# Optimization experiments

Measured on AMD Instinct MI355X. Metric: run time of the kernel, lower is better.

## Reference

```python
import jax, jax.numpy as jnp
import numpy as np

N = 50000; E = 800000; G = 64
HID = 128; HEADS = 4; HC = HID // HEADS
L = 3; RESID_FREQ = 2
EPS = 1e-5; SLOPE = 0.2


def setup_inputs() -> dict:
    key = jax.random.key(0)
    ks = jax.random.split(key, 16)
    s = 1.0 / np.sqrt(HID)
    f = jnp.float32
    return {
        "x": jax.random.normal(ks[0], (N, HID), f),
        "edge_index": jax.random.randint(ks[1], (2, E), 0, N, dtype=jnp.int32),
        "batch": jnp.sort(jax.random.randint(ks[2], (N,), 0, G, dtype=jnp.int32)),
        "w_in1": jax.random.normal(ks[3], (HID, HID), f) * s,
        "b_in1": jnp.zeros((HID,), f),
        "w_in2": jax.random.normal(ks[4], (HID, HID), f) * s,
        "b_in2": jnp.zeros((HID,), f),
        "gat_w": jax.random.normal(ks[5], (L, HID, HID), f) * s,
        "gat_att_src": jax.random.normal(ks[6], (L, HEADS, HC), f) * s,
        "gat_att_dst": jax.random.normal(ks[7], (L, HEADS, HC), f) * s,
        "gat_b": jnp.zeros((L, HID), f),
        "gcn_w": jax.random.normal(ks[8], (L, HID, HID), f) * s,
        "gcn_b": jnp.zeros((L, HID), f),
        "norm_w": jnp.ones((L, HID), f),
        "norm_b": jnp.zeros((L, HID), f),
        "norm_ms": jnp.ones((L, HID), f),
        "skip_w": jax.random.normal(ks[9], (L, HID, HID), f) * s,
        "skip_b": jnp.zeros((L, HID), f),
        "w_h1": jax.random.normal(ks[10], (HID, HID), f) * s,
        "b_h1": jnp.zeros((HID,), f),
        "w_h2": jax.random.normal(ks[11], (HID, HID // 2), f) * s,
        "b_h2": jnp.zeros((HID // 2,), f),
        "w_h3": jax.random.normal(ks[12], (HID // 2, 1), f) * s,
        "b_h3": jnp.zeros((1,), f),
        "edge_w_param": jnp.ones((1,), f),
    }


def _gat(x, src, dst, w, a_src, a_dst, b):
    # PyG GATConv (eval): lin -> per-edge additive attention -> edge softmax over dst -> scatter-sum
    h = (x @ w).reshape(N, HEADS, HC)
    sc_src = jnp.sum(h * a_src, axis=-1)  # [N, H]
    sc_dst = jnp.sum(h * a_dst, axis=-1)
    alpha = jax.nn.leaky_relu(sc_src[src] + sc_dst[dst], SLOPE)  # [Ef, H]
    amax = jax.ops.segment_max(alpha, dst, num_segments=N)  # every node has a self-loop
    ex = jnp.exp(alpha - amax[dst])
    denom = jax.ops.segment_sum(ex, dst, num_segments=N)
    coef = ex / (denom[dst] + 1e-16)
    out = jax.ops.segment_sum(h[src] * coef[:, :, None], dst, num_segments=N)
    return out.reshape(N, HID) + b


def _gcn(x, src, dst, ew, w, b):
    # PyG GCNConv with improved=True (self-loop weight 2.0 already in ew): sym-normalized SpMM
    deg = jax.ops.segment_sum(ew, dst, num_segments=N)
    dinv = jnp.where(deg > 0, jax.lax.rsqrt(deg), 0.0)
    norm = dinv[src] * ew * dinv[dst]
    h = x @ w
    return jax.ops.segment_sum(h[src] * norm[:, None], dst, num_segments=N) + b


def _graph_norm(x, batch, w, b, ms):
    cnt = jax.ops.segment_sum(jnp.ones((N, 1), x.dtype), batch, num_segments=G)
    cnt = jnp.maximum(cnt, 1.0)
    mean = jax.ops.segment_sum(x, batch, num_segments=G) / cnt
    out = x - mean[batch] * ms
    var = jax.ops.segment_sum(out * out, batch, num_segments=G) / cnt
    return out / jnp.sqrt(var[batch] + EPS) * w + b


def reference(x, edge_index, batch, w_in1, b_in1, w_in2, b_in2, gat_w, gat_att_src,
              gat_att_dst, gat_b, gcn_w, gcn_b, norm_w, norm_b, norm_ms, skip_w,
              skip_b, w_h1, b_h1, w_h2, b_h2, w_h3, b_h3, edge_w_param):
    # undirected: concat reversed edges; then self-loops (added by both GAT and GCN convs)
    loop = jnp.arange(N, dtype=edge_index.dtype)
    src = jnp.concatenate([edge_index[0], edge_index[1], loop])
    dst = jnp.concatenate([edge_index[1], edge_index[0], loop])
    ew = jnp.concatenate([
        edge_w_param[0] * jnp.ones((2 * E,), x.dtype),
        2.0 * jnp.ones((N,), x.dtype),  # improved=True self-loop fill value
    ])
    h = jax.nn.relu(x @ w_in1 + b_in1) @ w_in2 + b_in2
    for i in range(L):
        prev = h
        g1 = _gat(h, src, dst, gat_w[i], gat_att_src[i], gat_att_dst[i], gat_b[i])
        g2 = _gcn(h, src, dst, ew, gcn_w[i], gcn_b[i])
        h = jax.nn.elu(_graph_norm(g1 + g2, batch, norm_w[i], norm_b[i], norm_ms[i]))
        if i % RESID_FREQ == 0:
            h = h + prev @ skip_w[i] + skip_b[i]
    p = jax.nn.relu(h @ w_h1 + b_h1)
    p = jax.nn.relu(p @ w_h2 + b_h2)
    return jax.nn.sigmoid(p @ w_h3 + b_h3).reshape(-1)
```

## Files before the change

kernel.cpp:

```cpp
#include <hip/hip_runtime.h>
#include <hip/hip_fp16.h>

typedef unsigned int uint;
typedef unsigned short ushort;
typedef __attribute__((ext_vector_type(8))) short short8;
typedef __attribute__((ext_vector_type(4))) float f32x4;
typedef __attribute__((ext_vector_type(2))) float f32x2;

#define N_NODES 50000
#define N_EDGES 800000
#define EREAL   (2 * N_EDGES)
#define ETOT    (2 * N_EDGES + N_NODES)
#define NG      64
#define NBKT    256
#define MAXB    10240
#define EPB     8192
#define NBK1    ((EREAL + EPB - 1) / EPB)
#define AROW    640

__device__ __forceinline__ short f2bf(float f) {
  uint u = __float_as_uint(f);
  u += 0x7fffu + ((u >> 16) & 1u);
  return (short)(u >> 16);
}
__device__ __forceinline__ float bf2f(short s) {
  return __uint_as_float(((uint)(ushort)s) << 16);
}
__device__ __forceinline__ uint packbf(float a, float b) {
  return (uint)(ushort)f2bf(a) | ((uint)(ushort)f2bf(b) << 16);
}
__device__ __forceinline__ uint pkh2(float a, float b) {
  __half2 h = __floats2half2_rn(a, b);
  return *(uint*)&h;
}
__device__ __forceinline__ float2 uph2(uint u) {
  __half2 h = *(__half2*)&u;
  return __half22float2(h);
}

__global__ __launch_bounds__(256) void bucket_k(const int* __restrict__ ei,
                                                int* __restrict__ gfill,
                                                uint* __restrict__ est) {
  __shared__ int hist[NBKT];
  __shared__ int scan_[NBKT];
  __shared__ int cur[NBKT];
  __shared__ int claim[NBKT];
  __shared__ int wsum[4];
  __shared__ uint stage[EPB];
  const int tid = threadIdx.x;
  hist[tid] = 0;
  __syncthreads();
  const int e0 = blockIdx.x * EPB;
  const int ecnt = min(EPB, EREAL - e0);
  for (int i = tid; i < ecnt; i += 256) {
    int e = e0 + i;
    int d = (e < N_EDGES) ? ei[N_EDGES + e] : ei[e - N_EDGES];
    atomicAdd(&hist[d >> 8], 1);
  }
  __syncthreads();
  {
    int v = hist[tid];
    int lane = tid & 63, wid = tid >> 6;
    int x = v;
#pragma unroll
    for (int d = 1; d < 64; d <<= 1) {
      int t = __shfl_up(x, d, 64);
      if (lane >= d) x += t;
    }
    if (lane == 63) wsum[wid] = x;
    __syncthreads();
    int woff = 0;
#pragma unroll
    for (int j = 0; j < 4; ++j) if (j < wid) woff += wsum[j];
    scan_[tid] = woff + x - v;
    cur[tid] = woff + x - v;
    claim[tid] = atomicAdd(&gfill[tid], v);
  }
  __syncthreads();
  for (int i = tid; i < ecnt; i += 256) {
    int e = e0 + i;
    int s = ei[e];
    int d = (e < N_EDGES) ? ei[N_EDGES + e] : ei[e - N_EDGES];
    int p = atomicAdd(&cur[d >> 8], 1);
    stage[p] = (uint)s | ((uint)d << 16);
  }
  __syncthreads();
  for (int p = tid; p < ecnt; p += 256) {
    uint en = stage[p];
    int b = en >> 24;
    int gpos = claim[b] + (p - scan_[b]);
    est[(size_t)b * MAXB + gpos] = en;
  }
}

__global__ __launch_bounds__(256) void group_k(const int* __restrict__ gfill,
                                               const uint* __restrict__ est,
                                               const float* __restrict__ ewp,
                                               int* __restrict__ csrc,
                                               int* __restrict__ rbeg,
                                               int* __restrict__ rend,
                                               float* __restrict__ dinv) {
  __shared__ int hist[NBKT];
  __shared__ int cursor[NBKT];
  __shared__ int wsum[4];
  __shared__ int bsum[4];
  const int b = blockIdx.x;
  const int tid = threadIdx.x;
  const int lane = tid & 63, wid = tid >> 6;
  const int cnt = gfill[b];
  {
    int vv = (tid < b) ? gfill[tid] : 0;
#pragma unroll
    for (int off = 32; off; off >>= 1) vv += __shfl_xor(vv, off, 64);
    if (lane == 0) bsum[wid] = vv;
  }
  hist[tid] = 0;
  __syncthreads();
  const int gb = bsum[0] + bsum[1] + bsum[2] + bsum[3] + b * 256;
  const uint* basep = est + (size_t)b * MAXB;
  for (int i = tid; i < cnt; i += 256)
    atomicAdd(&hist[(basep[i] >> 16) & 255], 1);
  __syncthreads();
  int v = hist[tid];
  int x = v;
#pragma unroll
  for (int d = 1; d < 64; d <<= 1) {
    int t = __shfl_up(x, d, 64);
    if (lane >= d) x += t;
  }
  if (lane == 63) wsum[wid] = x;
  __syncthreads();
  int woff = 0;
#pragma unroll
  for (int j = 0; j < 4; ++j) if (j < wid) woff += wsum[j];
  int excl = woff + x - v;
  cursor[tid] = excl + tid + 1;
  int node = b * 256 + tid;
  if (node < N_NODES) {
    int rs = gb + excl + tid;
    rbeg[node] = rs;
    rend[node] = rs + v + 1;
    csrc[rs] = node | (int)0x80000000;
    float deg = ewp[0] * (float)v + 2.0f;
    dinv[node] = (deg > 0.f) ? rsqrtf(deg) : 0.f;
  }
  __syncthreads();
  for (int i = tid; i < cnt; i += 256) {
    uint en = basep[i];
    int dlow = (en >> 16) & 255;
    int slot = atomicAdd(&cursor[dlow], 1);
    csrc[gb + slot] = (int)(en & 0xffffu);
  }
}

__global__ __launch_bounds__(256) void prepall_k(const float* __restrict__ w_in1,
                                                 const float* __restrict__ w_in2,
                                                 const float* __restrict__ gat_w,
                                                 const float* __restrict__ gcn_w,
                                                 const float* __restrict__ skip_w,
                                                 const float* __restrict__ w_h1,
                                                 const float* __restrict__ w_h2,
                                                 const float* __restrict__ asrc,
                                                 const float* __restrict__ adst,
                                                 const float* __restrict__ gat_b,
                                                 const float* __restrict__ gcn_b,
                                                 const int* __restrict__ batch,
                                                 short* __restrict__ WT0,
                                                 short* __restrict__ WT1,
                                                 short* __restrict__ WTL2,
                                                 short* __restrict__ WTS,
                                                 short* __restrict__ WTH1,
                                                 short* __restrict__ WTH2,
                                                 short* __restrict__ ATTW,
                                                 float* __restrict__ BSUM,
                                                 int* __restrict__ gcnt) {
  __shared__ int lb[NG + 1];
  const int tid = threadIdx.x;
  if (blockIdx.x == 48) {
    for (int t = tid; t < 3072; t += 256) {
      int l = t >> 10, rem = t & 1023;
      int r = rem >> 7, k = rem & 127;
      int hd = r & 3;
      const float* av = (r < 4) ? (asrc + l * 128 + hd * 32) : (adst + l * 128 + hd * 32);
      const float* wrow = gat_w + (size_t)l * 16384 + k * 128 + hd * 32;
      float s = 0.f;
#pragma unroll
      for (int c = 0; c < 32; ++c) s = fmaf(wrow[c], av[c], s);
      ATTW[(size_t)l * 2048 + r * 128 + k] = f2bf(s);
    }
    for (int t = tid; t < 3072; t += 256)
      ATTW[(size_t)(t >> 10) * 2048 + 1024 + (t & 1023)] = 0;
    for (int t = tid; t < 384; t += 256) {
      int l = t >> 7, c = t & 127;
      BSUM[t] = gat_b[l * 128 + c] + gcn_b[l * 128 + c];
    }
    return;
  }
  if (blockIdx.x == 49) {
    int g = tid;
    if (g <= NG) {
      int lo = 0, hi = N_NODES;
      while (lo < hi) {
        int mid = (lo + hi) >> 1;
        if (batch[mid] < g) lo = mid + 1; else hi = mid;
      }
      lb[g] = lo;
    }
    __syncthreads();
    if (g < NG) gcnt[g] = lb[g + 1] - lb[g];
    return;
  }
  int mat = blockIdx.x >> 2, qr = blockIdx.x & 3;
  const float* src; short* dst; int ncol = 128, dstride = 128, doff = 0;
  switch (mat) {
    case 0:  src = w_in1; dst = WT0; break;
    case 1:  src = w_in2; dst = WT1; break;
    case 2: case 3: case 4:
      src = gat_w + (size_t)(mat - 2) * 16384; dst = WTL2 + (size_t)(mat - 2) * 32768;
      dstride = 256; break;
    case 5: case 6: case 7:
      src = gcn_w + (size_t)(mat - 5) * 16384; dst = WTL2 + (size_t)(mat - 5) * 32768;
      dstride = 256; doff = 128; break;
    case 8:  src = skip_w;             dst = WTS;         break;
    case 9:  src = skip_w + 2 * 16384; dst = WTS + 16384; break;
    case 10: src = w_h1; dst = WTH1; break;
    default: src = w_h2; dst = WTH2; ncol = 64; break;
  }
  int total = 128 * ncol, chunk = total / 4;
  for (int d = qr * chunk + tid; d < (qr + 1) * chunk; d += 256) {
    int col = d >> 7, k = d & 127;
    dst[col * dstride + doff + k] = f2bf(src[k * ncol + col]);
  }
}

template <int NCOL, int RELU, int F32OUT, int NORM>
__global__ __launch_bounds__(256) void bgemm_k(const short* __restrict__ A,
                                               const short* __restrict__ WT,
                                               const float* __restrict__ bias,
                                               const short* __restrict__ gb_,
                                               const int* __restrict__ batch,
                                               const int* __restrict__ gcnt,
                                               const float* __restrict__ gsum,
                                               const float* __restrict__ nw,
                                               const float* __restrict__ nb_,
                                               const float* __restrict__ nms,
                                               short* __restrict__ outb,
                                               float* __restrict__ outf, int M) {
  constexpr int NT = NCOL / 16;
  const int lane = threadIdx.x & 63;
  const int wid = threadIdx.x >> 6;
  const int mbase = blockIdx.x * 64 + wid * 16;
  const int l15 = lane & 15, q = lane >> 4;
  int arow = mbase + l15; if (arow > M - 1) arow = M - 1;
  const short* ap = A + (size_t)arow * 128 + q * 8;
  const short* bp = WT + (size_t)l15 * 128 + q * 8;
  f32x4 acc[NT];
#pragma unroll
  for (int t = 0; t < NT; ++t) acc[t] = (f32x4)0.f;
#pragma unroll
  for (int c = 0; c < 4; ++c) {
    short8 av = *(const short8*)(ap + c * 32);
#pragma unroll
    for (int t = 0; t < NT; ++t) {
      short8 bv = *(const short8*)(bp + (size_t)t * 16 * 128 + c * 32);
      acc[t] = __builtin_amdgcn_mfma_f32_16x16x32_bf16(av, bv, acc[t], 0, 0, 0);
    }
  }
#pragma unroll
  for (int t = 0; t < NT; ++t) {
    int col = t * 16 + l15;
    float bb = bias ? bias[col] : 0.f;
#pragma unroll
    for (int r = 0; r < 4; ++r) {
      int row = mbase + q * 4 + r;
      if (row < M) {
        float v = acc[t][r] + bb;
        if (NORM) {
          int b = batch[row];
          float cinv = 1.0f / fmaxf((float)gcnt[b], 1.0f);
          float mean = gsum[b * 256 + col] * cinv;
          float msq  = gsum[b * 256 + 128 + col] * cinv;
          float ms = nms[col];
          float var = fmaxf(msq - (2.0f * ms - ms * ms) * mean * mean, 0.f);
          float g = bf2f(gb_[(size_t)row * AROW + col]);
          float tn = (g - mean * ms) * rsqrtf(var + 1e-5f) * nw[col] + nb_[col];
          tn = (tn > 0.f) ? tn : (__expf(tn) - 1.0f);
          v += tn;
        }
        if (RELU) v = v > 0.f ? v : 0.f;
        if (F32OUT) outf[(size_t)row * NCOL + col] = v;
        else        outb[(size_t)row * NCOL + col] = f2bf(v);
      }
    }
  }
}

__global__ __launch_bounds__(256) void mlp2_k(const float* __restrict__ x,
                                              const short* __restrict__ WT0,
                                              const float* __restrict__ b1,
                                              const short* __restrict__ WT1,
                                              const float* __restrict__ b2,
                                              short* __restrict__ outb, int M) {
  __shared__ short sh[64][136];
  const int lane = threadIdx.x & 63;
  const int wid = threadIdx.x >> 6;
  const int mbase = blockIdx.x * 64 + wid * 16;
  const int l15 = lane & 15, q = lane >> 4;
  int arow = mbase + l15; if (arow > M - 1) arow = M - 1;
  f32x4 acc[8];
#pragma unroll
  for (int t = 0; t < 8; ++t) acc[t] = (f32x4)0.f;
#pragma unroll
  for (int c = 0; c < 4; ++c) {
    const float* apf = x + (size_t)arow * 128 + q * 8 + c * 32;
    float4 fa = *(const float4*)apf;
    float4 fb = *(const float4*)(apf + 4);
    uint4 all = make_uint4(packbf(fa.x, fa.y), packbf(fa.z, fa.w),
                           packbf(fb.x, fb.y), packbf(fb.z, fb.w));
    short8 av = *(short8*)&all;
    const short* bp = WT0 + (size_t)l15 * 128 + q * 8 + c * 32;
#pragma unroll
    for (int t = 0; t < 8; ++t) {
      short8 bv = *(const short8*)(bp + (size_t)t * 16 * 128);
      acc[t] = __builtin_amdgcn_mfma_f32_16x16x32_bf16(av, bv, acc[t], 0, 0, 0);
    }
  }
#pragma unroll
  for (int t = 0; t < 8; ++t) {
    int col = t * 16 + l15;
    float bb = b1[col];
#pragma unroll
    for (int r = 0; r < 4; ++r) {
      float v = acc[t][r] + bb;
      sh[wid * 16 + q * 4 + r][col] = f2bf(v > 0.f ? v : 0.f);
    }
  }
  __syncthreads();
  f32x4 acc2[8];
#pragma unroll
  for (int t = 0; t < 8; ++t) acc2[t] = (f32x4)0.f;
  const short* ap2 = &sh[wid * 16 + l15][0] + q * 8;
#pragma unroll
  for (int c = 0; c < 4; ++c) {
    short8 av = *(const short8*)(ap2 + c * 32);
    const short* bp = WT1 + (size_t)l15 * 128 + q * 8 + c * 32;
#pragma unroll
    for (int t = 0; t < 8; ++t) {
      short8 bv = *(const short8*)(bp + (size_t)t * 16 * 128);
      acc2[t] = __builtin_amdgcn_mfma_f32_16x16x32_bf16(av, bv, acc2[t], 0, 0, 0);
    }
  }
#pragma unroll
  for (int t = 0; t < 8; ++t) {
    int col = t * 16 + l15;
    float bb = b2[col];
#pragma unroll
    for (int r = 0; r < 4; ++r) {
      int row = mbase + q * 4 + r;
      if (row < M) outb[(size_t)row * 128 + col] = f2bf(acc2[t][r] + bb);
    }
  }
}

__global__ __launch_bounds__(256) void head_k(const short* __restrict__ h,
                                              const short* __restrict__ WTH1,
                                              const float* __restrict__ b1,
                                              const short* __restrict__ WTH2,
                                              const float* __restrict__ b2,
                                              const float* __restrict__ w3,
                                              const float* __restrict__ b3,
                                              float* __restrict__ out, int M) {
  __shared__ short sh[64][136];
  const int lane = threadIdx.x & 63;
  const int wid = threadIdx.x >> 6;
  const int mbase = blockIdx.x * 64 + wid * 16;
  const int l15 = lane & 15, q = lane >> 4;
  int arow = mbase + l15; if (arow > M - 1) arow = M - 1;
  const short* ap = h + (size_t)arow * 128 + q * 8;
  f32x4 acc[8];
#pragma unroll
  for (int t = 0; t < 8; ++t) acc[t] = (f32x4)0.f;
#pragma unroll
  for (int c = 0; c < 4; ++c) {
    short8 av = *(const short8*)(ap + c * 32);
    const short* bp = WTH1 + (size_t)l15 * 128 + q * 8 + c * 32;
#pragma unroll
    for (int t = 0; t < 8; ++t) {
      short8 bv = *(const short8*)(bp + (size_t)t * 16 * 128);
      acc[t] = __builtin_amdgcn_mfma_f32_16x16x32_bf16(av, bv, acc[t], 0, 0, 0);
    }
  }
#pragma unroll
  for (int t = 0; t < 8; ++t) {
    int col = t * 16 + l15;
    float bb = b1[col];
#pragma unroll
    for (int r = 0; r < 4; ++r) {
      float v = acc[t][r] + bb;
      sh[wid * 16 + q * 4 + r][col] = f2bf(v > 0.f ? v : 0.f);
    }
  }
  __syncthreads();
  f32x4 p2[4];
#pragma unroll
  for (int t = 0; t < 4; ++t) p2[t] = (f32x4)0.f;
  const short* ap2 = &sh[wid * 16 + l15][0] + q * 8;
#pragma unroll
  for (int c = 0; c < 4; ++c) {
    short8 av = *(const short8*)(ap2 + c * 32);
    const short* bp = WTH2 + (size_t)l15 * 128 + q * 8 + c * 32;
#pragma unroll
    for (int t = 0; t < 4; ++t) {
      short8 bv = *(const short8*)(bp + (size_t)t * 16 * 128);
      p2[t] = __builtin_amdgcn_mfma_f32_16x16x32_bf16(av, bv, p2[t], 0, 0, 0);
    }
  }
  float w3v[4];
#pragma unroll
  for (int t = 0; t < 4; ++t) w3v[t] = w3[t * 16 + l15];
  float rsum[4];
#pragma unroll
  for (int r = 0; r < 4; ++r) {
    float s = 0.f;
#pragma unroll
    for (int t = 0; t < 4; ++t) {
      float v = p2[t][r] + b2[t * 16 + l15];
      v = v > 0.f ? v : 0.f;
      s = fmaf(v, w3v[t], s);
    }
    rsum[r] = s;
  }
#pragma unroll
  for (int off = 1; off < 16; off <<= 1)
#pragma unroll
    for (int r = 0; r < 4; ++r) rsum[r] += __shfl_xor(rsum[r], off, 64);
  if (l15 == 0) {
#pragma unroll
    for (int r = 0; r < 4; ++r) {
      int row = mbase + q * 4 + r;
      if (row < M) out[row] = 1.0f / (1.0f + __expf(-(rsum[r] + b3[0])));
    }
  }
}

__global__ __launch_bounds__(256) void agg_k(const short* __restrict__ h,
                                             const float* __restrict__ sc,
                                             const int* __restrict__ rbeg,
                                             const int* __restrict__ rend,
                                             const int* __restrict__ cs,
                                             const float* __restrict__ dinv,
                                             const float* __restrict__ ewp,
                                             short* __restrict__ A) {
  __shared__ uint4 lco[4][64];
  const int n = blockIdx.x * 4 + (threadIdx.x >> 6);
  const int wv = threadIdx.x >> 6;
  const int l = threadIdx.x & 63;
  const int sub = l >> 5;
  const int f4 = l & 31;
  const float ew0 = ewp[0];
  const float dn = dinv[n];
  const f32x4 sdv = *(const f32x4*)(sc + n * 16 + 4);
  const int beg = rbeg[n], end = rend[n];
  float den[4] = {0.f, 0.f, 0.f, 0.f};
  f32x2 ag[4][2], ac[2];
#pragma unroll
  for (int hd = 0; hd < 4; ++hd) { ag[hd][0] = (f32x2)0.f; ag[hd][1] = (f32x2)0.f; }
  ac[0] = (f32x2)0.f; ac[1] = (f32x2)0.f;

  for (int c0 = beg; c0 < end; c0 += 64) {
    const int nc = min(64, end - c0);
    {
      uint4 w = make_uint4(0u, 0u, 0u, 0u);
      int e = c0 + l;
      if (e < end) {
        int raw = cs[e];
        int s = raw & 0x7fffffff;
        float wt = (raw < 0) ? 2.0f : ew0;
        f32x4 ssv = *(const f32x4*)(sc + (size_t)s * 16);
        float a0 = ssv[0] + sdv[0]; a0 = fmaxf(a0, 0.2f * a0);
        float a1 = ssv[1] + sdv[1]; a1 = fmaxf(a1, 0.2f * a1);
        float a2 = ssv[2] + sdv[2]; a2 = fmaxf(a2, 0.2f * a2);
        float a3 = ssv[3] + sdv[3]; a3 = fmaxf(a3, 0.2f * a3);
        float e0 = __expf(a0), e1 = __expf(a1);
        float e2 = __expf(a2), e3 = __expf(a3);
        den[0] += e0; den[1] += e1; den[2] += e2; den[3] += e3;
        float c2 = dinv[s] * wt * dn;
        __half hc = __float2half(c2);
        w = make_uint4(pkh2(e0, e1), pkh2(e2, e3),
                       (uint)(*(ushort*)&hc) | ((uint)s << 16), 0u);
      }
      lco[wv][l] = w;
    }
    const int pairs = (nc + 1) & ~1;
#pragma unroll 2
    for (int j = sub; j < pairs; j += 2) {
      uint4 cw = lco[wv][j];
      int s = (int)(cw.z >> 16);
      float2 p01 = uph2(cw.x);
      float2 p23 = uph2(cw.y);
      ushort hc = (ushort)(cw.z & 0xffffu);
      float c2 = __half2float(*(__half*)&hc);
      uint2 u = *(const uint2*)(h + (size_t)s * 128 + f4 * 4);
      f32x2 va, vb;
      va.x = __uint_as_float(u.x << 16);
      va.y = __uint_as_float(u.x & 0xffff0000u);
      vb.x = __uint_as_float(u.y << 16);
      vb.y = __uint_as_float(u.y & 0xffff0000u);
      f32x2 cc;
      cc.x = p01.x; cc.y = p01.x;
      ag[0][0] += cc * va; ag[0][1] += cc * vb;
      cc.x = p01.y; cc.y = p01.y;
      ag[1][0] += cc * va; ag[1][1] += cc * vb;
      cc.x = p23.x; cc.y = p23.x;
      ag[2][0] += cc * va; ag[2][1] += cc * vb;
      cc.x = p23.y; cc.y = p23.y;
      ag[3][0] += cc * va; ag[3][1] += cc * vb;
      cc.x = c2; cc.y = c2;
      ac[0] += cc * va; ac[1] += cc * vb;
    }
  }

#pragma unroll
  for (int off = 1; off < 64; off <<= 1) {
    den[0] += __shfl_xor(den[0], off, 64);
    den[1] += __shfl_xor(den[1], off, 64);
    den[2] += __shfl_xor(den[2], off, 64);
    den[3] += __shfl_xor(den[3], off, 64);
  }
#pragma unroll
  for (int hd = 0; hd < 4; ++hd)
#pragma unroll
    for (int i = 0; i < 2; ++i) {
      f32x2 t = ag[hd][i];
      t.x += __shfl_xor(t.x, 32, 64);
      t.y += __shfl_xor(t.y, 32, 64);
      ag[hd][i] = t;
    }
#pragma unroll
  for (int i = 0; i < 2; ++i) {
    f32x2 t = ac[i];
    t.x += __shfl_xor(t.x, 32, 64);
    t.y += __shfl_xor(t.y, 32, 64);
    ac[i] = t;
  }

  float inv[4] = {1.0f / (den[0] + 1e-16f), 1.0f / (den[1] + 1e-16f),
                  1.0f / (den[2] + 1e-16f), 1.0f / (den[3] + 1e-16f)};
  short* base = A + (size_t)n * AROW;
  if (sub == 0) {
#pragma unroll
    for (int hd = 0; hd < 2; ++hd) {
      float iv = inv[hd];
      *(uint2*)(base + hd * 128 + f4 * 4) =
          make_uint2(packbf(ag[hd][0].x * iv, ag[hd][0].y * iv),
                     packbf(ag[hd][1].x * iv, ag[hd][1].y * iv));
    }
    *(uint2*)(base + 512 + f4 * 4) =
        make_uint2(packbf(ac[0].x, ac[0].y), packbf(ac[1].x, ac[1].y));
  } else {
#pragma unroll
    for (int hd = 2; hd < 4; ++hd) {
      float iv = inv[hd];
      *(uint2*)(base + hd * 128 + f4 * 4) =
          make_uint2(packbf(ag[hd][0].x * iv, ag[hd][0].y * iv),
                     packbf(ag[hd][1].x * iv, ag[hd][1].y * iv));
    }
  }
}

__global__ __launch_bounds__(256) void aggproj_k(const short* A,
                                                 const short* __restrict__ WT,
                                                 const float* __restrict__ bsum,
                                                 short* GB, int M) {
  const int lane = threadIdx.x & 63;
  const int wid = threadIdx.x >> 6;
  const int mbase = blockIdx.x * 64 + wid * 16;
  const int l15 = lane & 15, q = lane >> 4;
  int arow = mbase + l15; if (arow > M - 1) arow = M - 1;
  const short* ap = A + (size_t)arow * AROW + q * 8;
  const short* bp = WT + (size_t)l15 * 256 + q * 8;
  f32x4 acc[8];
#pragma unroll
  for (int t = 0; t < 8; ++t) acc[t] = (f32x4)0.f;
  short8 avg[4];
#pragma unroll
  for (int c = 0; c < 4; ++c) avg[c] = *(const short8*)(ap + 512 + c * 32);
#pragma unroll
  for (int hd = 0; hd < 4; ++hd) {
    short8 avh[4];
#pragma unroll
    for (int c = 0; c < 4; ++c) avh[c] = *(const short8*)(ap + hd * 128 + c * 32);
#pragma unroll
    for (int tt = 0; tt < 2; ++tt) {
      int t = hd * 2 + tt;
      const short* bpt = bp + (size_t)t * 16 * 256;
#pragma unroll
      for (int c = 0; c < 4; ++c) {
        short8 bv = *(const short8*)(bpt + c * 32);
        acc[t] = __builtin_amdgcn_mfma_f32_16x16x32_bf16(avh[c], bv, acc[t], 0, 0, 0);
      }
#pragma unroll
      for (int c = 0; c < 4; ++c) {
        short8 bv = *(const short8*)(bpt + 128 + c * 32);
        acc[t] = __builtin_amdgcn_mfma_f32_16x16x32_bf16(avg[c], bv, acc[t], 0, 0, 0);
      }
    }
  }
#pragma unroll
  for (int t = 0; t < 8; ++t) {
    int col = t * 16 + l15;
    float bb = bsum[col];
#pragma unroll
    for (int r = 0; r < 4; ++r) {
      int row = mbase + q * 4 + r;
      if (row < M) GB[(size_t)row * AROW + col] = f2bf(acc[t][r] + bb);
    }
  }
}

__global__ __launch_bounds__(256) void stats_k(const short* __restrict__ gb,
                                               const int* __restrict__ batch,
                                               float* __restrict__ gsum) {
  int c2 = threadIdx.x & 63;
  int qr = threadIdx.x >> 6;
  int nb = blockIdx.x * 16;
  float s0 = 0.f, s1 = 0.f, q0 = 0.f, q1 = 0.f;
  int curb = -1;
  for (int i = qr; i < 16; i += 4) {
    int n = nb + i;
    int b = batch[n];
    if (b != curb) {
      if (curb >= 0) {
        atomicAdd(&gsum[curb * 256 + 2 * c2], s0);
        atomicAdd(&gsum[curb * 256 + 2 * c2 + 1], s1);
        atomicAdd(&gsum[curb * 256 + 128 + 2 * c2], q0);
        atomicAdd(&gsum[curb * 256 + 128 + 2 * c2 + 1], q1);
      }
      curb = b; s0 = s1 = q0 = q1 = 0.f;
    }
    uint u = *(const uint*)(gb + (size_t)n * AROW + 2 * c2);
    float v0 = __uint_as_float(u << 16);
    float v1 = __uint_as_float(u & 0xffff0000u);
    s0 += v0; q0 = fmaf(v0, v0, q0);
    s1 += v1; q1 = fmaf(v1, v1, q1);
  }
  if (curb >= 0) {
    atomicAdd(&gsum[curb * 256 + 2 * c2], s0);
    atomicAdd(&gsum[curb * 256 + 2 * c2 + 1], s1);
    atomicAdd(&gsum[curb * 256 + 128 + 2 * c2], q0);
    atomicAdd(&gsum[curb * 256 + 128 + 2 * c2 + 1], q1);
  }
}

__global__ __launch_bounds__(256) void normelu_k(const short* __restrict__ gb,
                                                 const int* __restrict__ batch,
                                                 const float* __restrict__ gsum,
                                                 const int* __restrict__ gcnt,
                                                 const float* __restrict__ nw,
                                                 const float* __restrict__ nb_,
                                                 const float* __restrict__ nms,
                                                 short* __restrict__ outb) {
  int n = blockIdx.x * 4 + (threadIdx.x >> 6);
  int c2 = threadIdx.x & 63;
  int b = batch[n];
  float cntf = fmaxf((float)gcnt[b], 1.0f);
  float cinv = 1.0f / cntf;
  uint u = *(const uint*)(gb + (size_t)n * AROW + 2 * c2);
  float o[2];
#pragma unroll
  for (int k = 0; k < 2; ++k) {
    int c = 2 * c2 + k;
    float mean = gsum[b * 256 + c] * cinv;
    float msq  = gsum[b * 256 + 128 + c] * cinv;
    float ms = nms[c];
    float var = fmaxf(msq - (2.0f * ms - ms * ms) * mean * mean, 0.f);
    float v = (k == 0) ? __uint_as_float(u << 16) : __uint_as_float(u & 0xffff0000u);
    float t = (v - mean * ms) * rsqrtf(var + 1e-5f) * nw[c] + nb_[c];
    o[k] = (t > 0.f) ? t : (__expf(t) - 1.0f);
  }
  *(uint*)(outb + (size_t)n * 128 + 2 * c2) = packbf(o[0], o[1]);
}

extern "C" void kernel_launch(void* const* d_in, const int* in_sizes, int n_in,
                              void* d_out, int out_size, void* d_ws, size_t ws_size,
                              hipStream_t stream) {
  const float* x      = (const float*)d_in[0];
  const int*   ei     = (const int*)d_in[1];
  const int*   batch  = (const int*)d_in[2];
  const float* w_in1  = (const float*)d_in[3];
  const float* b_in1  = (const float*)d_in[4];
  const float* w_in2  = (const float*)d_in[5];
  const float* b_in2  = (const float*)d_in[6];
  const float* gat_w  = (const float*)d_in[7];
  const float* gat_as = (const float*)d_in[8];
  const float* gat_ad = (const float*)d_in[9];
  const float* gat_b  = (const float*)d_in[10];
  const float* gcn_w  = (const float*)d_in[11];
  const float* gcn_b  = (const float*)d_in[12];
  const float* norm_w = (const float*)d_in[13];
  const float* norm_b = (const float*)d_in[14];
  const float* norm_ms= (const float*)d_in[15];
  const float* skip_w = (const float*)d_in[16];
  const float* skip_b = (const float*)d_in[17];
  const float* w_h1   = (const float*)d_in[18];
  const float* b_h1   = (const float*)d_in[19];
  const float* w_h2   = (const float*)d_in[20];
  const float* b_h2   = (const float*)d_in[21];
  const float* w_h3   = (const float*)d_in[22];
  const float* b_h3   = (const float*)d_in[23];
  const float* ewp    = (const float*)d_in[24];
  float* out = (float*)d_out;

  char* p = (char*)d_ws;
  const size_t NBH = (size_t)N_NODES * 128 * sizeof(short);
  short* B0   = (short*)p; p += NBH;
  short* B1   = (short*)p; p += NBH;
  short* MEGA = (short*)p; p += (size_t)N_NODES * AROW * sizeof(short);
  short* GB   = MEGA;
  uint*  EST  = (uint*)MEGA;
  float* SC   = (float*)p; p += (size_t)N_NODES * 16 * sizeof(float);
  int*   CSRC = (int*)p;   p += (size_t)ETOT * sizeof(int);
  int*   RBEG = (int*)p;   p += (size_t)N_NODES * sizeof(int);
  int*   REND = (int*)p;   p += (size_t)N_NODES * sizeof(int);
  char*  zbase = p;
  int*   GFILL= (int*)p;   p += (size_t)NBKT * sizeof(int);
  float* GSUM = (float*)p; p += (size_t)3 * NG * 256 * sizeof(float);
  size_t znb  = (size_t)((char*)p - zbase);
  int*   GCNT = (int*)p;   p += (size_t)NG * sizeof(int);
  float* DINV = (float*)p; p += (size_t)N_NODES * sizeof(float);
  short* WT0  = (short*)p; p += 16384 * sizeof(short);
  short* WT1  = (short*)p; p += 16384 * sizeof(short);
  short* WTL2 = (short*)p; p += 3 * 32768 * sizeof(short);
  short* WTS  = (short*)p; p += 2 * 16384 * sizeof(short);
  short* WTH1 = (short*)p; p += 16384 * sizeof(short);
  short* WTH2 = (short*)p; p += 8192 * sizeof(short);
  short* ATTW = (short*)p; p += 3 * 2048 * sizeof(short);
  float* BSUM = (float*)p; p += 3 * 128 * sizeof(float);

  const int GB_ = (N_NODES + 63) / 64;
  const short* nullb = nullptr;

  hipMemsetAsync(zbase, 0, znb, stream);
  bucket_k<<<NBK1, 256, 0, stream>>>(ei, GFILL, EST);
  group_k<<<196, 256, 0, stream>>>(GFILL, EST, ewp, CSRC, RBEG, REND, DINV);
  prepall_k<<<50, 256, 0, stream>>>(w_in1, w_in2, gat_w, gcn_w, skip_w, w_h1,
                                    w_h2, gat_as, gat_ad, gat_b, gcn_b, batch,
                                    WT0, WT1, WTL2, WTS, WTH1, WTH2, ATTW,
                                    BSUM, GCNT);

  mlp2_k<<<GB_, 256, 0, stream>>>(x, WT0, b_in1, WT1, b_in2, B0, N_NODES);

  short* h = B0;
  for (int i = 0; i < 3; ++i) {
    short* hn = (h == B0) ? B1 : B0;
    float* gsum_i = GSUM + (size_t)i * NG * 256;
    const float* nw  = norm_w  + (size_t)i * 128;
    const float* nb  = norm_b  + (size_t)i * 128;
    const float* nms = norm_ms + (size_t)i * 128;
    bgemm_k<16, 0, 1, 0><<<GB_, 256, 0, stream>>>(h, ATTW + (size_t)i * 2048,
        nullptr, nullb, nullptr, nullptr, nullptr, nullptr, nullptr, nullptr,
        nullptr, SC, N_NODES);
    agg_k<<<N_NODES / 4, 256, 0, stream>>>(h, SC, RBEG, REND, CSRC, DINV, ewp, MEGA);
    aggproj_k<<<GB_, 256, 0, stream>>>(MEGA, WTL2 + (size_t)i * 32768,
                                       BSUM + i * 128, GB, N_NODES);
    stats_k<<<N_NODES / 16, 256, 0, stream>>>(GB, batch, gsum_i);
    if (i == 1) {
      normelu_k<<<N_NODES / 4, 256, 0, stream>>>(GB, batch, gsum_i, GCNT,
                                                 nw, nb, nms, hn);
    } else {
      const short* wts = WTS + (size_t)(i == 0 ? 0 : 1) * 16384;
      bgemm_k<128, 0, 0, 1><<<GB_, 256, 0, stream>>>(h, wts,
          skip_b + (size_t)i * 128, GB, batch, GCNT, gsum_i, nw, nb, nms,
          hn, nullptr, N_NODES);
    }
    h = hn;
  }

  head_k<<<GB_, 256, 0, stream>>>(h, WTH1, b_h1, WTH2, b_h2, w_h3, b_h3, out,
                                  N_NODES);
}
```

Baseline: 813.3 us.

## Compute graph-norm stats per graph block without atomics using segment offsets

The stats kernel now launches one block per graph and uses precomputed graph offsets (written by the prep kernel) to sum each graph's contiguous node range. Partial sums are combined in shared memory and written directly, so the global atomics and the GSUM memset go away. The cost is far less parallelism: 64 blocks, each streaming about 780 rows serially with four rows in flight per step, which may leave most of the GPU idle.

Result: slower. 893.4 us (+9.8%).

```diff
diff --git a/kernel.cpp b/kernel.cpp
--- a/kernel.cpp
+++ b/kernel.cpp
@@ -173,7 +173,8 @@
                                                  short* __restrict__ WTH2,
                                                  short* __restrict__ ATTW,
                                                  float* __restrict__ BSUM,
-                                                 int* __restrict__ gcnt) {
+                                                 int* __restrict__ gcnt,
+                                                 int* __restrict__ goff) {
   __shared__ int lb[NG + 1];
   const int tid = threadIdx.x;
   if (blockIdx.x == 48) {
@@ -205,6 +206,7 @@
         if (batch[mid] < g) lo = mid + 1; else hi = mid;
       }
       lb[g] = lo;
+      goff[g] = lo;
     }
     __syncthreads();
     if (g < NG) gcnt[g] = lb[g + 1] - lb[g];
@@ -619,37 +621,30 @@
 }
 
 __global__ __launch_bounds__(256) void stats_k(const short* __restrict__ gb,
-                                               const int* __restrict__ batch,
+                                               const int* __restrict__ goff,
                                                float* __restrict__ gsum) {
-  int c2 = threadIdx.x & 63;
-  int qr = threadIdx.x >> 6;
-  int nb = blockIdx.x * 16;
+  __shared__ float red[4][512];
+  const int g = blockIdx.x;
+  const int c2 = threadIdx.x & 63;
+  const int qr = threadIdx.x >> 6;
+  const int lo = goff[g], hi = goff[g + 1];
   float s0 = 0.f, s1 = 0.f, q0 = 0.f, q1 = 0.f;
-  int curb = -1;
-  for (int i = qr; i < 16; i += 4) {
-    int n = nb + i;
-    int b = batch[n];
-    if (b != curb) {
-      if (curb >= 0) {
-        atomicAdd(&gsum[curb * 256 + 2 * c2], s0);
-        atomicAdd(&gsum[curb * 256 + 2 * c2 + 1], s1);
-        atomicAdd(&gsum[curb * 256 + 128 + 2 * c2], q0);
-        atomicAdd(&gsum[curb * 256 + 128 + 2 * c2 + 1], q1);
-      }
-      curb = b; s0 = s1 = q0 = q1 = 0.f;
-    }
+  for (int n = lo + qr; n < hi; n += 4) {
     uint u = *(const uint*)(gb + (size_t)n * AROW + 2 * c2);
     float v0 = __uint_as_float(u << 16);
     float v1 = __uint_as_float(u & 0xffff0000u);
     s0 += v0; q0 = fmaf(v0, v0, q0);
     s1 += v1; q1 = fmaf(v1, v1, q1);
   }
-  if (curb >= 0) {
-    atomicAdd(&gsum[curb * 256 + 2 * c2], s0);
-    atomicAdd(&gsum[curb * 256 + 2 * c2 + 1], s1);
-    atomicAdd(&gsum[curb * 256 + 128 + 2 * c2], q0);
-    atomicAdd(&gsum[curb * 256 + 128 + 2 * c2 + 1], q1);
-  }
+  red[qr][2 * c2] = s0;
+  red[qr][2 * c2 + 1] = s1;
+  red[qr][256 + 2 * c2] = q0;
+  red[qr][256 + 2 * c2 + 1] = q1;
+  __syncthreads();
+  int kind = threadIdx.x >> 7, f = threadIdx.x & 127;
+  float v = red[0][kind * 256 + f] + red[1][kind * 256 + f] +
+            red[2][kind * 256 + f] + red[3][kind * 256 + f];
+  gsum[g * 256 + kind * 128 + f] = v;
 }
 
 __global__ __launch_bounds__(256) void normelu_k(const short* __restrict__ gb,
@@ -724,9 +719,10 @@
   int*   REND = (int*)p;   p += (size_t)N_NODES * sizeof(int);
   char*  zbase = p;
   int*   GFILL= (int*)p;   p += (size_t)NBKT * sizeof(int);
+  size_t znb  = (size_t)((char*)p - zbase);
   float* GSUM = (float*)p; p += (size_t)3 * NG * 256 * sizeof(float);
-  size_t znb  = (size_t)((char*)p - zbase);
   int*   GCNT = (int*)p;   p += (size_t)NG * sizeof(int);
+  int*   GOFF = (int*)p;   p += (size_t)(NG + 1) * sizeof(int);
   float* DINV = (float*)p; p += (size_t)N_NODES * sizeof(float);
   short* WT0  = (short*)p; p += 16384 * sizeof(short);
   short* WT1  = (short*)p; p += 16384 * sizeof(short);
@@ -746,7 +742,7 @@
   prepall_k<<<50, 256, 0, stream>>>(w_in1, w_in2, gat_w, gcn_w, skip_w, w_h1,
                                     w_h2, gat_as, gat_ad, gat_b, gcn_b, batch,
                                     WT0, WT1, WTL2, WTS, WTH1, WTH2, ATTW,
-                                    BSUM, GCNT);
+                                    BSUM, GCNT, GOFF);
 
   mlp2_k<<<GB_, 256, 0, stream>>>(x, WT0, b_in1, WT1, b_in2, B0, N_NODES);
 
@@ -763,7 +759,7 @@
     agg_k<<<N_NODES / 4, 256, 0, stream>>>(h, SC, RBEG, REND, CSRC, DINV, ewp, MEGA);
     aggproj_k<<<GB_, 256, 0, stream>>>(MEGA, WTL2 + (size_t)i * 32768,
                                        BSUM + i * 128, GB, N_NODES);
-    stats_k<<<N_NODES / 16, 256, 0, stream>>>(GB, batch, gsum_i);
+    stats_k<<<NG, 256, 0, stream>>>(GB, GOFF, gsum_i);
     if (i == 1) {
       normelu_k<<<N_NODES / 4, 256, 0, stream>>>(GB, batch, gsum_i, GCNT,
                                                  nw, nb, nms, hn);
```
